# Performance work log

Hardware: AMD Instinct MI355X
Metric: run time of the kernel (lower is better)

## Reference

```python
import jax, jax.numpy as jnp
import numpy as np

INPUT, OUTPUT, HIDDEN, EMBED = 20000, 2048, 1024, 512
BATCH, NUM_GENES = 512, 20000

def _linear_init(key, fan_in, fan_out):
    kw, kb = jax.random.split(key)
    bound = 1.0 / np.sqrt(fan_in)
    W = jax.random.uniform(kw, (fan_out, fan_in), minval=-bound, maxval=bound, dtype=jnp.float32)
    b = jax.random.uniform(kb, (fan_out,), minval=-bound, maxval=bound, dtype=jnp.float32)
    return W, b

def setup_inputs() -> dict:
    key = jax.random.key(0)
    kx, ke, k1, k2, k3 = jax.random.split(key, 5)
    x = jax.random.normal(kx, (BATCH, INPUT), dtype=jnp.float32)
    embedding_x = jax.random.normal(ke, (NUM_GENES, EMBED), dtype=jnp.float32)
    W_ge, b_ge = _linear_init(k1, INPUT, HIDDEN)   # gene_expander Linear
    W_em, b_em = _linear_init(k2, EMBED, HIDDEN)   # embed_mlp Linear
    W_c, b_c = _linear_init(k3, 2 * HIDDEN, OUTPUT)  # combiner Linear
    return {"x": x, "embedding_x": embedding_x, "W_ge": W_ge, "b_ge": b_ge,
            "W_em": W_em, "b_em": b_em, "W_c": W_c, "b_c": b_c}

def reference(x, embedding_x, W_ge, b_ge, W_em, b_em, W_c, b_c):
    lrelu = lambda v: jax.nn.leaky_relu(v, negative_slope=0.01)
    # gene_expander: [B, input] -> [B, hidden]
    x_expanded = lrelu(x @ W_ge.T + b_ge)
    # embed_mlp (dropout = identity at eval): [G, embed] -> [G, hidden]
    gene_embeddings = lrelu(embedding_x @ W_em.T + b_em)
    # softmax over features, then batched GEMM replaces the per-sample loop
    num_genes = min(x.shape[1], gene_embeddings.shape[0])
    weights = jax.nn.softmax(x, axis=1)
    weighted_embeddings = weights[:, :num_genes] @ gene_embeddings[:num_genes]  # [B, hidden]
    combined = jnp.concatenate([x_expanded, weighted_embeddings], axis=1)  # [B, 2*hidden]
    return lrelu(combined @ W_c.T + b_c)  # [B, output]
```

## Files before the change

### kernel.cpp

```cpp
#include <hip/hip_runtime.h>
#include <hip/hip_bf16.h>
#include <stdint.h>

#define BATCH  512
#define INPUT  20000
#define KPAD   20032
#define NPADE  20096
#define HIDDEN 1024
#define EMBED  512
#define NOUT   2048

typedef __attribute__((ext_vector_type(8))) __bf16 bf16x8;
typedef __attribute__((ext_vector_type(8))) unsigned short u16x8;
typedef __attribute__((ext_vector_type(4))) unsigned short u16x4;
typedef __attribute__((ext_vector_type(4))) float f32x4;

static __device__ __forceinline__ unsigned short f2bf(float f) {
  uint32_t u = __builtin_bit_cast(uint32_t, f);
  u += 0x7fffu + ((u >> 16) & 1u);
  return (unsigned short)(u >> 16);
}

static __device__ __forceinline__ void g2l16(const unsigned short* g, unsigned short* l) {
  __builtin_amdgcn_global_load_lds(
      (const __attribute__((address_space(1))) void*)g,
      (__attribute__((address_space(3))) void*)l, 16, 0, 0);
}

#define MFMA(a, b, c) __builtin_amdgcn_mfma_f32_16x16x32_bf16((a), (b), (c), 0, 0, 0)

__global__ __launch_bounds__(512, 2) void gemm8p_fused(
    const unsigned short* __restrict__ xb, const unsigned short* __restrict__ Wgeb,
    const unsigned short* __restrict__ wb, const unsigned short* __restrict__ Etp,
    float* __restrict__ P, int kChunk)
{
  __shared__ __align__(16) unsigned short As[2][2][128 * 64];
  __shared__ __align__(16) unsigned short Bs[2][2][128 * 64];
  unsigned short* AsW = &As[0][0][0];
  unsigned short* BsW = &Bs[0][0][0];

  const int which = blockIdx.z >> 4;
  const int z     = blockIdx.z & 15;
  const unsigned short* Ap = which ? wb  : xb;
  const unsigned short* Bp = which ? Etp : Wgeb;

  const int m0 = blockIdx.y * 256, n0 = blockIdx.x * 256;
  const int k0   = z * kChunk;
  const int kend = min(KPAD, k0 + kChunk);
  const int nt   = (kend - k0) >> 6;

  const int tid = threadIdx.x;
  const int l = tid & 63, w = tid >> 6;
  const int srow = tid >> 3, scol = (tid & 7) * 8;

  const unsigned short* ag = Ap + (size_t)(m0 + srow) * KPAD + k0 + scol;
  const unsigned short* bg = Bp + (size_t)(n0 + srow) * KPAD + k0 + scol;

  const int wr = w >> 2, wc = w & 3;
  const int lr = l & 15, lk = (l >> 4) * 8;

  auto stA = [&](int buf, int h, int dk) {
    const unsigned short* g = ag + (size_t)(h * 128) * KPAD + dk;
    unsigned short* d = AsW + (buf * 2 + h) * 8192 + (w * 8) * 64;
    g2l16(g, d);
    g2l16(g + (size_t)64 * KPAD, d + 64 * 64);
  };
  auto stB = [&](int buf, int h, int dk) {
    const unsigned short* g = bg + (size_t)(h * 128) * KPAD + dk;
    unsigned short* d = BsW + (buf * 2 + h) * 8192 + (w * 8) * 64;
    g2l16(g, d);
    g2l16(g + (size_t)64 * KPAD, d + 64 * 64);
  };
  auto rdA = [&](int buf, int mi, int ks) -> bf16x8 {
    return *reinterpret_cast<const bf16x8*>(
        AsW + (buf * 2 + wr) * 8192 + (mi * 16 + lr) * 64 + ks * 32 + lk);
  };
  auto rdB = [&](int buf, int ni, int ks) -> bf16x8 {
    return *reinterpret_cast<const bf16x8*>(
        BsW + (buf * 2 + (wc >> 1)) * 8192 + ((wc & 1) * 64 + ni * 16 + lr) * 64 + ks * 32 + lk);
  };

  f32x4 acc[8][4] = {};

  stA(0, 0, 0); stB(0, 0, 0); stA(0, 1, 0); stB(0, 1, 0);
  if (nt > 1) {
    stA(1, 0, 64); stB(1, 0, 64);
    asm volatile("s_waitcnt vmcnt(4)" ::: "memory");
  } else {
    asm volatile("s_waitcnt vmcnt(0)" ::: "memory");
  }
  __builtin_amdgcn_s_barrier();

  for (int t = 0; t < nt; ++t) {
    const int buf = t & 1, nb = buf ^ 1;
    const int dk1 = (t + 1) << 6, dk2 = (t + 2) << 6;
    bf16x8 a0[4][2], a1[4][2], b0[2][2], b1[2][2];

#pragma unroll
    for (int mi = 0; mi < 4; ++mi) { a0[mi][0] = rdA(buf, mi, 0); a0[mi][1] = rdA(buf, mi, 1); }
#pragma unroll
    for (int ni = 0; ni < 2; ++ni) { b0[ni][0] = rdB(buf, ni, 0); b0[ni][1] = rdB(buf, ni, 1); }
    if (t + 1 < nt) stA(nb, 1, dk1);
    __builtin_amdgcn_s_barrier();
    asm volatile("s_waitcnt lgkmcnt(0)" ::: "memory");
    __builtin_amdgcn_sched_barrier(0);
    __builtin_amdgcn_s_setprio(1);
#pragma unroll
    for (int mi = 0; mi < 4; ++mi)
#pragma unroll
      for (int ni = 0; ni < 2; ++ni) {
        acc[mi][ni] = MFMA(a0[mi][0], b0[ni][0], acc[mi][ni]);
        acc[mi][ni] = MFMA(a0[mi][1], b0[ni][1], acc[mi][ni]);
      }
    __builtin_amdgcn_s_setprio(0);
    __builtin_amdgcn_s_barrier();

#pragma unroll
    for (int mi = 0; mi < 4; ++mi) { a1[mi][0] = rdA(buf, mi + 4, 0); a1[mi][1] = rdA(buf, mi + 4, 1); }
    if (t + 1 < nt) stB(nb, 1, dk1);
    __builtin_amdgcn_s_barrier();
    asm volatile("s_waitcnt lgkmcnt(0)" ::: "memory");
    __builtin_amdgcn_sched_barrier(0);
    __builtin_amdgcn_s_setprio(1);
#pragma unroll
    for (int mi = 0; mi < 4; ++mi)
#pragma unroll
      for (int ni = 0; ni < 2; ++ni) {
        acc[mi + 4][ni] = MFMA(a1[mi][0], b0[ni][0], acc[mi + 4][ni]);
        acc[mi + 4][ni] = MFMA(a1[mi][1], b0[ni][1], acc[mi + 4][ni]);
      }
    __builtin_amdgcn_s_setprio(0);
    __builtin_amdgcn_s_barrier();

#pragma unroll
    for (int ni = 0; ni < 2; ++ni) { b1[ni][0] = rdB(buf, ni + 2, 0); b1[ni][1] = rdB(buf, ni + 2, 1); }
    if (t + 2 < nt) stA(buf, 0, dk2);
    __builtin_amdgcn_s_barrier();
    asm volatile("s_waitcnt lgkmcnt(0)" ::: "memory");
    __builtin_amdgcn_sched_barrier(0);
    __builtin_amdgcn_s_setprio(1);
#pragma unroll
    for (int mi = 0; mi < 4; ++mi)
#pragma unroll
      for (int ni = 0; ni < 2; ++ni) {
        acc[mi + 4][ni + 2] = MFMA(a1[mi][0], b1[ni][0], acc[mi + 4][ni + 2]);
        acc[mi + 4][ni + 2] = MFMA(a1[mi][1], b1[ni][1], acc[mi + 4][ni + 2]);
      }
    __builtin_amdgcn_s_setprio(0);
    __builtin_amdgcn_s_barrier();

    if (t + 2 < nt) stB(buf, 0, dk2);
    __builtin_amdgcn_s_barrier();
    __builtin_amdgcn_sched_barrier(0);
    __builtin_amdgcn_s_setprio(1);
#pragma unroll
    for (int mi = 0; mi < 4; ++mi)
#pragma unroll
      for (int ni = 0; ni < 2; ++ni) {
        acc[mi][ni + 2] = MFMA(a0[mi][0], b1[ni][0], acc[mi][ni + 2]);
        acc[mi][ni + 2] = MFMA(a0[mi][1], b1[ni][1], acc[mi][ni + 2]);
      }
    __builtin_amdgcn_s_setprio(0);
    if (t + 2 < nt)      asm volatile("s_waitcnt vmcnt(4)" ::: "memory");
    else if (t + 1 < nt) asm volatile("s_waitcnt vmcnt(0)" ::: "memory");
    __builtin_amdgcn_s_barrier();
  }

  const int rb = (l >> 4) * 4;
  float* dst = P + (size_t)z * (BATCH * NOUT) + which * 1024;
#pragma unroll
  for (int mi = 0; mi < 8; ++mi)
#pragma unroll
    for (int ni = 0; ni < 4; ++ni)
#pragma unroll
      for (int j = 0; j < 4; ++j) {
        int m = m0 + wr * 128 + mi * 16 + rb + j;
        int n = n0 + wc * 64 + ni * 16 + lr;
        dst[(size_t)m * NOUT + n] = acc[mi][ni][j];
      }
}

template<int EPI>
__global__ __launch_bounds__(256) void gemm97(
    const unsigned short* __restrict__ A, const unsigned short* __restrict__ B,
    int lda, int ldb,
    const float* __restrict__ bias,
    void* __restrict__ Cp, int ldc, int pstride,
    int M, int N, int Nw, int K, int kChunk)
{
  __shared__ __align__(16) unsigned short As[128 * 64];
  __shared__ __align__(16) unsigned short Bs[128 * 64];

  const int z = blockIdx.z;
  const int m0 = blockIdx.y * 128, n0 = blockIdx.x * 128;
  const int k0   = z * kChunk;
  const int kend = min(K, k0 + kChunk);
  const int tid = threadIdx.x;
  const int l = tid & 63, w = tid >> 6;

  const int srow = w * 32 + (l >> 3);
  const int scol = (l & 7) * 8;
  const unsigned short* ag = A + (size_t)(m0 + srow) * lda + scol;
  const unsigned short* bg = B + (size_t)(n0 + srow) * ldb + scol;

  const int wm = (w >> 1) * 64, wn = (w & 1) * 64;
  const int lr = l & 15, lk = (l >> 4) * 8;

  f32x4 acc[4][4] = {};

  for (int kb = k0; kb < kend; kb += 64) {
#pragma unroll
    for (int j = 0; j < 4; ++j)
      g2l16(ag + (size_t)j * 8 * lda + kb, As + (w * 32 + j * 8) * 64);
#pragma unroll
    for (int j = 0; j < 4; ++j)
      g2l16(bg + (size_t)j * 8 * ldb + kb, Bs + (w * 32 + j * 8) * 64);
    __syncthreads();
#pragma unroll
    for (int ks = 0; ks < 2; ++ks) {
      bf16x8 a[4], b[4];
#pragma unroll
      for (int i = 0; i < 4; ++i)
        a[i] = *reinterpret_cast<const bf16x8*>(&As[(wm + i * 16 + lr) * 64 + ks * 32 + lk]);
#pragma unroll
      for (int i = 0; i < 4; ++i)
        b[i] = *reinterpret_cast<const bf16x8*>(&Bs[(wn + i * 16 + lr) * 64 + ks * 32 + lk]);
#pragma unroll
      for (int mi = 0; mi < 4; ++mi)
#pragma unroll
        for (int ni = 0; ni < 4; ++ni)
          acc[mi][ni] = MFMA(a[mi], b[ni], acc[mi][ni]);
    }
    __syncthreads();
  }

  const int rb = (l >> 4) * 4;
#pragma unroll
  for (int mi = 0; mi < 4; ++mi) {
#pragma unroll
    for (int ni = 0; ni < 4; ++ni) {
#pragma unroll
      for (int j = 0; j < 4; ++j) {
        int m = m0 + wm + mi * 16 + rb + j;
        int n = n0 + wn + ni * 16 + lr;
        float v = acc[mi][ni][j];
        if (EPI == 0) {
          if (n < Nw) {
            float t = v + bias[m];
            t = t > 0.f ? t : 0.01f * t;
            reinterpret_cast<unsigned short*>(Cp)[(size_t)m * ldc + n] =
                (n < N) ? f2bf(t) : (unsigned short)0;
          }
        } else {
          reinterpret_cast<float*>(Cp)[(size_t)z * pstride + (size_t)m * ldc + n] = v;
        }
      }
    }
  }
}

__global__ __launch_bounds__(256) void convert_kernel(
    const float* __restrict__ src, unsigned short* __restrict__ dst,
    int rows, int cols, int rowsPad, int colsPad)
{
  const int cpc = colsPad >> 3;
  const int nchunks = rowsPad * cpc;
  for (int idx = blockIdx.x * 256 + threadIdx.x; idx < nchunks; idx += gridDim.x * 256) {
    int row = idx / cpc;
    int c0  = (idx - row * cpc) << 3;
    u16x8 v = {};
    if (row < rows && c0 < cols) {
      const float* p = src + (size_t)row * cols + c0;
      f32x4 f0 = *reinterpret_cast<const f32x4*>(p);
      f32x4 f1 = *reinterpret_cast<const f32x4*>(p + 4);
      v[0] = f2bf(f0[0]); v[1] = f2bf(f0[1]); v[2] = f2bf(f0[2]); v[3] = f2bf(f0[3]);
      v[4] = f2bf(f1[0]); v[5] = f2bf(f1[1]); v[6] = f2bf(f1[2]); v[7] = f2bf(f1[3]);
    }
    *reinterpret_cast<u16x8*>(dst + (size_t)row * colsPad + c0) = v;
  }
}

__global__ __launch_bounds__(256) void prep_x_kernel(
    const float* __restrict__ x,
    unsigned short* __restrict__ xb,
    unsigned short* __restrict__ wb)
{
  const int r = blockIdx.x;
  const int t = threadIdx.x;
  const float* xr = x + (size_t)r * INPUT;

  float m = -3.4e38f, s = 0.f;
  for (int c = t; c < INPUT / 4; c += 256) {
    float4 v = reinterpret_cast<const float4*>(xr)[c];
    float cm = fmaxf(fmaxf(v.x, v.y), fmaxf(v.z, v.w));
    if (cm > m) { s *= __expf(m - cm); m = cm; }
    s += __expf(v.x - m) + __expf(v.y - m) + __expf(v.z - m) + __expf(v.w - m);
  }
#pragma unroll
  for (int off = 32; off > 0; off >>= 1) {
    float om = __shfl_xor(m, off);
    float os = __shfl_xor(s, off);
    float nm = fmaxf(m, om);
    s = s * __expf(m - nm) + os * __expf(om - nm);
    m = nm;
  }
  __shared__ float sm[4], ss[4];
  if ((t & 63) == 0) { sm[t >> 6] = m; ss[t >> 6] = s; }
  __syncthreads();
  float M4 = fmaxf(fmaxf(sm[0], sm[1]), fmaxf(sm[2], sm[3]));
  float S4 = ss[0] * __expf(sm[0] - M4) + ss[1] * __expf(sm[1] - M4)
           + ss[2] * __expf(sm[2] - M4) + ss[3] * __expf(sm[3] - M4);
  float inv = 1.f / S4;

  unsigned short* xbr = xb + (size_t)r * KPAD;
  unsigned short* wbr = wb + (size_t)r * KPAD;
  for (int c = t; c < KPAD / 4; c += 256) {
    u16x4 xo = {}, wo = {};
    if (c < INPUT / 4) {
      float4 v = reinterpret_cast<const float4*>(xr)[c];
      xo[0] = f2bf(v.x); xo[1] = f2bf(v.y); xo[2] = f2bf(v.z); xo[3] = f2bf(v.w);
      wo[0] = f2bf(__expf(v.x - M4) * inv);
      wo[1] = f2bf(__expf(v.y - M4) * inv);
      wo[2] = f2bf(__expf(v.z - M4) * inv);
      wo[3] = f2bf(__expf(v.w - M4) * inv);
    }
    reinterpret_cast<u16x4*>(xbr)[c] = xo;
    reinterpret_cast<u16x4*>(wbr)[c] = wo;
  }
}

template<int S, int MODE>
__global__ __launch_bounds__(256) void reduce_kernel(
    const float* __restrict__ P, const float* __restrict__ bias, void* __restrict__ outp)
{
  size_t base = ((size_t)blockIdx.x * 256 + threadIdx.x) * 4;
  f32x4 s = {};
#pragma unroll
  for (int zz = 0; zz < S; ++zz)
    s += *reinterpret_cast<const f32x4*>(P + (size_t)zz * BATCH * NOUT + base);
  int n = (int)(base & (NOUT - 1));
  if (MODE == 0) {
    u16x4 o;
    if (n < 1024) {
#pragma unroll
      for (int j = 0; j < 4; ++j) {
        float v = s[j] + bias[n + j];
        v = v > 0.f ? v : 0.01f * v;
        o[j] = f2bf(v);
      }
    } else {
#pragma unroll
      for (int j = 0; j < 4; ++j) o[j] = f2bf(s[j]);
    }
    *reinterpret_cast<u16x4*>(reinterpret_cast<unsigned short*>(outp) + base) = o;
  } else {
    f32x4 o;
#pragma unroll
    for (int j = 0; j < 4; ++j) {
      float v = s[j] + bias[n + j];
      o[j] = v > 0.f ? v : 0.01f * v;
    }
    *reinterpret_cast<f32x4*>(reinterpret_cast<float*>(outp) + base) = o;
  }
}

extern "C" void kernel_launch(void* const* d_in, const int* in_sizes, int n_in,
                              void* d_out, int out_size, void* d_ws, size_t ws_size,
                              hipStream_t stream)
{
  const float* x    = (const float*)d_in[0];
  const float* emb  = (const float*)d_in[1];
  const float* W_ge = (const float*)d_in[2];
  const float* b_ge = (const float*)d_in[3];
  const float* W_em = (const float*)d_in[4];
  const float* b_em = (const float*)d_in[5];
  const float* W_c  = (const float*)d_in[6];
  const float* b_c  = (const float*)d_in[7];
  float* out = (float*)d_out;

  char* ws = (char*)d_ws;
  unsigned short* xb   = (unsigned short*)(ws);
  unsigned short* wb   = (unsigned short*)(ws + 20512768);
  unsigned short* Wgeb = (unsigned short*)(ws + 41025536);
  unsigned short* Et   = (unsigned short*)(ws + 82051072);
  unsigned short* Wcb  = (unsigned short*)(ws + 123076608);
  unsigned short* comb = (unsigned short*)(ws + 131465216);
  float*          P    = (float*)(ws + 133562368);
  unsigned short* embb = (unsigned short*)(ws + 133562368);
  unsigned short* Wemb = (unsigned short*)(ws + 133562368 + 20578304);

  convert_kernel<<<1024, 256, 0, stream>>>(emb,  embb, INPUT, EMBED, NPADE, EMBED);
  convert_kernel<<<256,  256, 0, stream>>>(W_em, Wemb, HIDDEN, EMBED, HIDDEN, EMBED);
  convert_kernel<<<1024, 256, 0, stream>>>(W_ge, Wgeb, HIDDEN, INPUT, HIDDEN, KPAD);
  convert_kernel<<<512,  256, 0, stream>>>(W_c,  Wcb,  NOUT, NOUT, NOUT, NOUT);

  prep_x_kernel<<<BATCH, 256, 0, stream>>>(x, xb, wb);

  gemm97<0><<<dim3(157, 8, 1), 256, 0, stream>>>(
      Wemb, embb, EMBED, EMBED, b_em,
      Et, KPAD, 0, HIDDEN, INPUT, KPAD, EMBED, EMBED);

  gemm8p_fused<<<dim3(4, 2, 32), 512, 0, stream>>>(xb, Wgeb, wb, Et, P, 1280);

  reduce_kernel<16, 0><<<(BATCH * NOUT / 4) / 256, 256, 0, stream>>>(P, b_ge, comb);

  gemm97<1><<<dim3(16, 4, 4), 256, 0, stream>>>(
      comb, Wcb, NOUT, NOUT, nullptr,
      P, NOUT, BATCH * NOUT, BATCH, NOUT, NOUT, NOUT, 512);

  reduce_kernel<4, 1><<<(BATCH * NOUT / 4) / 256, 256, 0, stream>>>(P, b_c, out);
}
```

Measured before the change: 242.6 us.

## Generalize 256x256 GEMM kernel, use it for embed GEMM, add XOR LDS swizzle

Turns the fused 256x256-tile split-K kernel into a template with an epilogue mode and uses it in place of the 128x128 gemm97 for the embedding MLP GEMM. That mode applies bias, leaky ReLU and the bf16 transposed store, which needs the embedding padding raised to a multiple of 256. It also adds an XOR swizzle to the shared-memory column layout on both the global-to-LDS loads and the fragment reads, to cut LDS bank conflicts. The cost is 316 large blocks for the embed GEMM and extra padded rows that must be converted and computed.

```diff
diff --git a/kernel.cpp b/kernel.cpp
--- a/kernel.cpp
+++ b/kernel.cpp
@@ -5,7 +5,7 @@
 #define BATCH  512
 #define INPUT  20000
 #define KPAD   20032
-#define NPADE  20096
+#define NPADE  20224
 #define HIDDEN 1024
 #define EMBED  512
 #define NOUT   2048
@@ -29,55 +29,64 @@
 
 #define MFMA(a, b, c) __builtin_amdgcn_mfma_f32_16x16x32_bf16((a), (b), (c), 0, 0, 0)
 
-__global__ __launch_bounds__(512, 2) void gemm8p_fused(
-    const unsigned short* __restrict__ xb, const unsigned short* __restrict__ Wgeb,
-    const unsigned short* __restrict__ wb, const unsigned short* __restrict__ Etp,
-    float* __restrict__ P, int kChunk)
+template<int EPI>
+__global__ __launch_bounds__(512, 2) void gemm8p(
+    const unsigned short* __restrict__ A0p, const unsigned short* __restrict__ B0p,
+    const unsigned short* __restrict__ A1p, const unsigned short* __restrict__ B1p,
+    int lda, int ldb,
+    const float* __restrict__ bias,
+    void* __restrict__ Cp, int ldc,
+    int Nv, int Nw, int K, int kChunk)
 {
   __shared__ __align__(16) unsigned short As[2][2][128 * 64];
   __shared__ __align__(16) unsigned short Bs[2][2][128 * 64];
   unsigned short* AsW = &As[0][0][0];
   unsigned short* BsW = &Bs[0][0][0];
 
-  const int which = blockIdx.z >> 4;
-  const int z     = blockIdx.z & 15;
-  const unsigned short* Ap = which ? wb  : xb;
-  const unsigned short* Bp = which ? Etp : Wgeb;
+  const int zall  = blockIdx.z;
+  const int which = (EPI == 1) ? (zall >> 4) : 0;
+  const int z     = (EPI == 1) ? (zall & 15) : 0;
+  const unsigned short* Ap = which ? A1p : A0p;
+  const unsigned short* Bp = which ? B1p : B0p;
 
   const int m0 = blockIdx.y * 256, n0 = blockIdx.x * 256;
   const int k0   = z * kChunk;
-  const int kend = min(KPAD, k0 + kChunk);
+  const int kend = min(K, k0 + kChunk);
   const int nt   = (kend - k0) >> 6;
 
   const int tid = threadIdx.x;
   const int l = tid & 63, w = tid >> 6;
-  const int srow = tid >> 3, scol = (tid & 7) * 8;
-
-  const unsigned short* ag = Ap + (size_t)(m0 + srow) * KPAD + k0 + scol;
-  const unsigned short* bg = Bp + (size_t)(n0 + srow) * KPAD + k0 + scol;
+  const int srow = tid >> 3;
+  const int scol = (((tid & 7) ^ (srow & 7)) << 3);
+
+  const unsigned short* ag = Ap + (size_t)(m0 + srow) * lda + k0 + scol;
+  const unsigned short* bg = Bp + (size_t)(n0 + srow) * ldb + k0 + scol;
 
   const int wr = w >> 2, wc = w & 3;
   const int lr = l & 15, lk = (l >> 4) * 8;
+  const int xorv = (lr & 7) * 8;
+  const int c0 = lk ^ xorv;
+  const int c1 = (32 + lk) ^ xorv;
 
   auto stA = [&](int buf, int h, int dk) {
-    const unsigned short* g = ag + (size_t)(h * 128) * KPAD + dk;
+    const unsigned short* g = ag + (size_t)(h * 128) * lda + dk;
     unsigned short* d = AsW + (buf * 2 + h) * 8192 + (w * 8) * 64;
     g2l16(g, d);
-    g2l16(g + (size_t)64 * KPAD, d + 64 * 64);
+    g2l16(g + (size_t)64 * lda, d + 64 * 64);
   };
   auto stB = [&](int buf, int h, int dk) {
-    const unsigned short* g = bg + (size_t)(h * 128) * KPAD + dk;
+    const unsigned short* g = bg + (size_t)(h * 128) * ldb + dk;
     unsigned short* d = BsW + (buf * 2 + h) * 8192 + (w * 8) * 64;
     g2l16(g, d);
-    g2l16(g + (size_t)64 * KPAD, d + 64 * 64);
+    g2l16(g + (size_t)64 * ldb, d + 64 * 64);
   };
   auto rdA = [&](int buf, int mi, int ks) -> bf16x8 {
     return *reinterpret_cast<const bf16x8*>(
-        AsW + (buf * 2 + wr) * 8192 + (mi * 16 + lr) * 64 + ks * 32 + lk);
+        AsW + (buf * 2 + wr) * 8192 + (mi * 16 + lr) * 64 + (ks ? c1 : c0));
   };
   auto rdB = [&](int buf, int ni, int ks) -> bf16x8 {
     return *reinterpret_cast<const bf16x8*>(
-        BsW + (buf * 2 + (wc >> 1)) * 8192 + ((wc & 1) * 64 + ni * 16 + lr) * 64 + ks * 32 + lk);
+        BsW + (buf * 2 + (wc >> 1)) * 8192 + ((wc & 1) * 64 + ni * 16 + lr) * 64 + (ks ? c1 : c0));
   };
 
   f32x4 acc[8][4] = {};
@@ -167,7 +176,6 @@
   }
 
   const int rb = (l >> 4) * 4;
-  float* dst = P + (size_t)z * (BATCH * NOUT) + which * 1024;
 #pragma unroll
   for (int mi = 0; mi < 8; ++mi)
 #pragma unroll
@@ -176,7 +184,18 @@
       for (int j = 0; j < 4; ++j) {
         int m = m0 + wr * 128 + mi * 16 + rb + j;
         int n = n0 + wc * 64 + ni * 16 + lr;
-        dst[(size_t)m * NOUT + n] = acc[mi][ni][j];
+        float v = acc[mi][ni][j];
+        if (EPI == 0) {
+          if (n < Nw) {
+            float t2 = v + bias[m];
+            t2 = t2 > 0.f ? t2 : 0.01f * t2;
+            reinterpret_cast<unsigned short*>(Cp)[(size_t)m * ldc + n] =
+                (n < Nv) ? f2bf(t2) : (unsigned short)0;
+          }
+        } else {
+          reinterpret_cast<float*>(Cp)[(size_t)z * (BATCH * NOUT) + (size_t)m * ldc +
+                                       which * 1024 + n] = v;
+        }
       }
 }
 
@@ -387,7 +406,7 @@
   unsigned short* comb = (unsigned short*)(ws + 131465216);
   float*          P    = (float*)(ws + 133562368);
   unsigned short* embb = (unsigned short*)(ws + 133562368);
-  unsigned short* Wemb = (unsigned short*)(ws + 133562368 + 20578304);
+  unsigned short* Wemb = (unsigned short*)(ws + 133562368 + 20709376);
 
   convert_kernel<<<1024, 256, 0, stream>>>(emb,  embb, INPUT, EMBED, NPADE, EMBED);
   convert_kernel<<<256,  256, 0, stream>>>(W_em, Wemb, HIDDEN, EMBED, HIDDEN, EMBED);
@@ -396,11 +415,13 @@
 
   prep_x_kernel<<<BATCH, 256, 0, stream>>>(x, xb, wb);
 
-  gemm97<0><<<dim3(157, 8, 1), 256, 0, stream>>>(
-      Wemb, embb, EMBED, EMBED, b_em,
-      Et, KPAD, 0, HIDDEN, INPUT, KPAD, EMBED, EMBED);
-
-  gemm8p_fused<<<dim3(4, 2, 32), 512, 0, stream>>>(xb, Wgeb, wb, Et, P, 1280);
+  gemm8p<0><<<dim3(79, 4, 1), 512, 0, stream>>>(
+      Wemb, embb, nullptr, nullptr, EMBED, EMBED, b_em,
+      Et, KPAD, INPUT, KPAD, EMBED, EMBED);
+
+  gemm8p<1><<<dim3(4, 2, 32), 512, 0, stream>>>(
+      xb, Wgeb, wb, Et, KPAD, KPAD, nullptr,
+      P, NOUT, 0, 0, KPAD, 1280);
 
   reduce_kernel<16, 0><<<(BATCH * NOUT / 4) / 256, 256, 0, stream>>>(P, b_ge, comb);
 
```

New measurement: 244.3 us. Within noise of the previous version (+0.7%).
